# Kernel optimization log

Measured on AMD Instinct MI355X. Metric: run time of the kernel, lower is better.

## Reference

```python
import jax, jax.numpy as jnp
import numpy as np

N = 100000
F_IN = 256
F_OUT = 64
E = 3200000
NEG_SLOPE = 0.2


def setup_inputs() -> dict:
    key = jax.random.key(0)
    k1, k2, k3, k4, k5 = jax.random.split(key, 5)
    x = jax.random.normal(k1, (N, F_IN), dtype=jnp.float32)
    edge_index = jax.random.randint(k2, (2, E), 0, N, dtype=jnp.int32)
    # GATConv params (heads=1): lin weight, att_src, att_dst, bias
    W = jax.random.normal(k3, (F_IN, F_OUT), dtype=jnp.float32) / np.sqrt(F_IN)
    att_src = jax.random.normal(k4, (F_OUT,), dtype=jnp.float32) / np.sqrt(F_OUT)
    att_dst = jax.random.normal(k5, (F_OUT,), dtype=jnp.float32) / np.sqrt(F_OUT)
    bias = jnp.zeros((F_OUT,), dtype=jnp.float32)
    return {"x": x, "edge_index": edge_index, "W": W,
            "att_src": att_src, "att_dst": att_dst, "bias": bias}


def reference(x, edge_index, W, att_src, att_dst, bias):
    n = x.shape[0]
    h = x @ W  # [N, F_OUT]
    # add self-loops (PyG default add_self_loops=True)
    loops = jnp.arange(n, dtype=edge_index.dtype)
    src = jnp.concatenate([edge_index[0], loops])  # message source j
    dst = jnp.concatenate([edge_index[1], loops])  # message target i
    # per-node attention halves
    a_src = h @ att_src  # [N]
    a_dst = h @ att_dst  # [N]
    e = a_src[src] + a_dst[dst]  # [E+N]
    e = jnp.where(e > 0, e, NEG_SLOPE * e)  # LeakyReLU(0.2)
    # softmax over edges grouped by target node
    e_max = jax.ops.segment_max(e, dst, num_segments=n)
    e_max = jnp.where(jnp.isfinite(e_max), e_max, 0.0)
    p = jnp.exp(e - e_max[dst])
    denom = jax.ops.segment_sum(p, dst, num_segments=n)
    alpha = p / (denom[dst] + 1e-16)  # [E+N]
    # scatter-aggregate weighted source features
    out = jax.ops.segment_sum(alpha[:, None] * h[src], dst, num_segments=n)
    return out + bias
```

## Files before the change

kernel.cpp:

```cpp
#include <hip/hip_runtime.h>
#include <hip/hip_bf16.h>
#include <math.h>

#define F_IN 256
#define F_OUT 64
#define NEG_SLOPE 0.2f
#define SHIFT 7
#define NPB 128
#define MAXK 1024
#define CAP 4608
#define OVF 4
#define GRID_B 256

__device__ __forceinline__ float bf2f(__hip_bfloat16 v) {
    return __bfloat162float(v);
}

__global__ __launch_bounds__(256) void gemm_kernel(
    const float* __restrict__ x, const float* __restrict__ W,
    const float* __restrict__ att_src, const float* __restrict__ att_dst,
    __hip_bfloat16* __restrict__ h16, float* __restrict__ a_src,
    float* __restrict__ a_dst, int N)
{
    __shared__ float sX[64][65];
    __shared__ float sPa[4][64];
    __shared__ float sPd[4][64];

    const int t = threadIdx.x;
    const int lane = t & 63;
    const int w = t >> 6;
    const int rowBase = blockIdx.x * 64;
    const int row = rowBase + lane;
    const int c0 = __builtin_amdgcn_readfirstlane(w * 16);

    float acc[16];
#pragma unroll
    for (int c = 0; c < 16; c++) acc[c] = 0.f;

    const int kq = t & 15;
    const int rr = t >> 4;

    for (int kc = 0; kc < F_IN / 64; kc++) {
#pragma unroll
        for (int p = 0; p < 4; p++) {
            int r = rr + p * 16;
            float4 v = make_float4(0.f, 0.f, 0.f, 0.f);
            if (rowBase + r < N)
                v = *(const float4*)&x[(size_t)(rowBase + r) * F_IN + kc * 64 + kq * 4];
            sX[kq * 4 + 0][r] = v.x;
            sX[kq * 4 + 1][r] = v.y;
            sX[kq * 4 + 2][r] = v.z;
            sX[kq * 4 + 3][r] = v.w;
        }
        __syncthreads();

        const float* Wc = W + (size_t)(kc * 64) * F_OUT + c0;
#pragma unroll 4
        for (int kk = 0; kk < 64; kk++) {
            float xv = sX[kk][lane];
            const float* wr = Wc + (size_t)kk * F_OUT;
#pragma unroll
            for (int c = 0; c < 16; c++)
                acc[c] = fmaf(xv, wr[c], acc[c]);
        }
        __syncthreads();
    }

    float asp = 0.f, adp = 0.f;
#pragma unroll
    for (int c = 0; c < 16; c++) {
        asp = fmaf(acc[c], att_src[c0 + c], asp);
        adp = fmaf(acc[c], att_dst[c0 + c], adp);
    }
    sPa[w][lane] = asp;
    sPd[w][lane] = adp;

    if (row < N) {
        __hip_bfloat16 tmp[16];
#pragma unroll
        for (int c = 0; c < 16; c++) tmp[c] = __float2bfloat16(acc[c]);
        int4* dst = (int4*)(h16 + (size_t)row * F_OUT + c0);
        dst[0] = ((int4*)tmp)[0];
        dst[1] = ((int4*)tmp)[1];
    }

    __syncthreads();
    if (w == 0 && row < N) {
        a_src[row] = sPa[0][lane] + sPa[1][lane] + sPa[2][lane] + sPa[3][lane];
        a_dst[row] = sPd[0][lane] + sPd[1][lane] + sPd[2][lane] + sPd[3][lane];
    }
}

__global__ __launch_bounds__(1024) void bucket_count_kernel(
    const int* __restrict__ dst, int* __restrict__ pbh, int E, int K, int R)
{
    __shared__ int s[MAXK];
    const int t = threadIdx.x;
    for (int b = t; b < K; b += 1024) s[b] = 0;
    __syncthreads();
    const int start = blockIdx.x * R;
    const int end = min(E, start + R);
    for (int e = start + t * 4; e < end; e += 4096) {
        if (e + 3 < end) {
            int4 d = *(const int4*)&dst[e];
            atomicAdd(&s[d.x >> SHIFT], 1);
            atomicAdd(&s[d.y >> SHIFT], 1);
            atomicAdd(&s[d.z >> SHIFT], 1);
            atomicAdd(&s[d.w >> SHIFT], 1);
        } else {
            for (int q = e; q < end; q++) atomicAdd(&s[dst[q] >> SHIFT], 1);
        }
    }
    __syncthreads();
    int* row = pbh + (size_t)blockIdx.x * K;
    for (int b = t; b < K; b += 1024) row[b] = s[b];
}

__global__ __launch_bounds__(64) void colscan_kernel(
    const int* __restrict__ pbh, int* __restrict__ cbase,
    int* __restrict__ btot, int K, int NBLK)
{
    const int k = blockIdx.x;
    const int lane = threadIdx.x;
    int v[4];
#pragma unroll
    for (int c = 0; c < 4; c++) {
        int b = c * 64 + lane;
        v[c] = (b < NBLK) ? pbh[(size_t)b * K + k] : 0;
    }
    int carry = 0;
#pragma unroll
    for (int c = 0; c < 4; c++) {
        int orig = v[c];
        int s = v[c];
#pragma unroll
        for (int off = 1; off < 64; off <<= 1) {
            int u = __shfl_up(s, off, 64);
            if (lane >= off) s += u;
        }
        int b = c * 64 + lane;
        if (b < NBLK) cbase[(size_t)b * K + k] = carry + s - orig;
        carry += __shfl(s, 63, 64);
    }
    if (lane == 0) btot[k] = carry;
}

__global__ __launch_bounds__(1024) void bbase_scan_kernel(
    const int* __restrict__ btot, int* __restrict__ bbase, int K, int E)
{
    __shared__ int s[1024];
    const int t = threadIdx.x;
    int v = (t < K) ? btot[t] : 0;
    s[t] = v;
    __syncthreads();
    for (int off = 1; off < 1024; off <<= 1) {
        int u = (t >= off) ? s[t - off] : 0;
        __syncthreads();
        s[t] += u;
        __syncthreads();
    }
    if (t < K) bbase[t] = s[t] - v;
    if (t == 0) bbase[K] = E;
}

__global__ __launch_bounds__(1024) void bin_kernel(
    const int* __restrict__ ei, const int* __restrict__ cbase,
    const int* __restrict__ bbase, int* __restrict__ rec, int E, int K, int R)
{
    __shared__ int cb[MAXK];
    const int t = threadIdx.x;
    const int start = blockIdx.x * R;
    const int end = min(E, start + R);
    const int* crow = cbase + (size_t)blockIdx.x * K;
    for (int b = t; b < K; b += 1024) cb[b] = bbase[b] + crow[b];
    __syncthreads();

    for (int e = start + t * 4; e < end; e += 4096) {
        if (e + 3 < end) {
            int4 jj = *(const int4*)&ei[e];
            int4 ii = *(const int4*)&ei[E + e];
            int p0 = atomicAdd(&cb[ii.x >> SHIFT], 1);
            int p1 = atomicAdd(&cb[ii.y >> SHIFT], 1);
            int p2 = atomicAdd(&cb[ii.z >> SHIFT], 1);
            int p3 = atomicAdd(&cb[ii.w >> SHIFT], 1);
            rec[p0] = jj.x | ((ii.x & (NPB - 1)) << 17);
            rec[p1] = jj.y | ((ii.y & (NPB - 1)) << 17);
            rec[p2] = jj.z | ((ii.z & (NPB - 1)) << 17);
            rec[p3] = jj.w | ((ii.w & (NPB - 1)) << 17);
        } else {
            for (int q = e; q < end; q++) {
                int j = ei[q], i = ei[E + q];
                int pos = atomicAdd(&cb[i >> SHIFT], 1);
                rec[pos] = j | ((i & (NPB - 1)) << 17);
            }
        }
    }
}

__global__ __launch_bounds__(256) void sort_kernel(
    int* __restrict__ rec, const int* __restrict__ bbase,
    int* __restrict__ row_ptr, int N, int E, int K)
{
    __shared__ int stage[CAP];
    __shared__ int deg[NPB];
    __shared__ int sval[NPB];
    __shared__ int base[NPB];
    __shared__ int cnt[NPB];
    const int t = threadIdx.x;
    const int b = blockIdx.x;
    const int s = bbase[b], e = bbase[b + 1];
    const int tot = e - s;
    const int nodeBase = b << SHIFT;
    const int nodes = min(NPB, N - nodeBase);

    if (t < NPB) deg[t] = 0;
    __syncthreads();

    int ovf[OVF];
    for (int r = t; r < tot; r += 256) {
        int m = rec[s + r];
        if (r < CAP) stage[r] = m;
        else { int k = (r - CAP) >> 8; if (k < OVF) ovf[k] = m; }
        atomicAdd(&deg[(m >> 17) & (NPB - 1)], 1);
    }
    __syncthreads();

    if (t < NPB) sval[t] = deg[t];
    __syncthreads();
    for (int off = 1; off < NPB; off <<= 1) {
        int v = (t < NPB && t >= off) ? sval[t - off] : 0;
        __syncthreads();
        if (t < NPB) sval[t] += v;
        __syncthreads();
    }
    if (t < NPB) {
        base[t] = sval[t] - deg[t];
        cnt[t] = 0;
        if (t < nodes) row_ptr[nodeBase + t] = s + base[t];
    }
    if (b == K - 1 && t == 0) row_ptr[N] = E;
    __syncthreads();

    for (int r = t; r < tot; r += 256) {
        int m = (r < CAP) ? stage[r] : ovf[(r - CAP) >> 8];
        int li = (m >> 17) & (NPB - 1);
        int rk = atomicAdd(&cnt[li], 1);
        rec[s + base[li] + rk] = m;
    }
}

__global__ __launch_bounds__(256) void node_kernel(
    const __hip_bfloat16* __restrict__ h16, const float* __restrict__ a_src,
    const float* __restrict__ a_dst, const int* __restrict__ row_ptr,
    const int* __restrict__ rec, const float* __restrict__ bias,
    float* __restrict__ out, int N)
{
    const int w = threadIdx.x >> 6;
    const int lane = threadIdx.x & 63;
    const int i = blockIdx.x * 4 + w;
    if (i >= N) return;

    const int s = row_ptr[i];
    const int e = row_ptr[i + 1];

    const float adst_i = a_dst[i];
    float vs = a_src[i] + adst_i;
    vs = fmaxf(vs, NEG_SLOPE * vs);
    const float pself = __expf(vs);
    float denl = (lane == 0) ? pself : 0.f;
    float acc = pself * bf2f(h16[(size_t)i * F_OUT + lane]);

    for (int k = s; k < e; k += 64) {
        const int cnt = min(64, e - k);
        int r = (lane < cnt) ? rec[k + lane] : 0;
        int j = r & 0x1FFFF;
        float v = a_src[j] + adst_i;
        v = fmaxf(v, NEG_SLOPE * v);
        float p = __expf(v);
        if (lane >= cnt) p = 0.f;
        denl += p;

        int u = 0;
        for (; u + 8 <= cnt; u += 8) {
            int ju[8]; float pu[8], g[8];
#pragma unroll
            for (int c = 0; c < 8; c++) {
                ju[c] = __shfl(j, u + c, 64);
                pu[c] = __shfl(p, u + c, 64);
            }
#pragma unroll
            for (int c = 0; c < 8; c++)
                g[c] = bf2f(h16[(size_t)ju[c] * F_OUT + lane]);
            asm volatile("" ::: "memory");
#pragma unroll
            for (int c = 0; c < 8; c++)
                acc = fmaf(pu[c], g[c], acc);
        }
        for (; u < cnt; u++) {
            int jc = __shfl(j, u, 64);
            float pc = __shfl(p, u, 64);
            acc = fmaf(pc, bf2f(h16[(size_t)jc * F_OUT + lane]), acc);
        }
    }

    float den = denl;
#pragma unroll
    for (int o = 32; o > 0; o >>= 1) den += __shfl_xor(den, o, 64);

    out[(size_t)i * F_OUT + lane] = acc / (den + 1e-16f) + bias[lane];
}

extern "C" void kernel_launch(void* const* d_in, const int* in_sizes, int n_in,
                              void* d_out, int out_size, void* d_ws, size_t ws_size,
                              hipStream_t stream)
{
    const float* x      = (const float*)d_in[0];
    const int*   ei     = (const int*)d_in[1];
    const float* W      = (const float*)d_in[2];
    const float* att_sr = (const float*)d_in[3];
    const float* att_ds = (const float*)d_in[4];
    const float* bias   = (const float*)d_in[5];
    float* out = (float*)d_out;

    const int N = in_sizes[0] / F_IN;
    const int E = in_sizes[1] / 2;
    const int K = (N + NPB - 1) >> SHIFT;
    const int R = (((E + GRID_B - 1) / GRID_B) + 3) & ~3;

    char* ws = (char*)d_ws;
    size_t off = 0;
    auto alloc = [&](size_t bytes) -> void* {
        void* p = ws + off;
        off = (off + bytes + 255) & ~(size_t)255;
        return p;
    };
    __hip_bfloat16* h16 = (__hip_bfloat16*)alloc((size_t)N * F_OUT * 2);
    float* a_src   = (float*)alloc((size_t)N * 4);
    float* a_dst   = (float*)alloc((size_t)N * 4);
    int*   pbh     = (int*)alloc((size_t)GRID_B * K * 4);
    int*   cbase   = (int*)alloc((size_t)GRID_B * K * 4);
    int*   btot    = (int*)alloc((size_t)K * 4);
    int*   bbase   = (int*)alloc((size_t)(K + 1) * 4);
    int*   row_ptr = (int*)alloc((size_t)(N + 1) * 4);
    int*   rec     = (int*)alloc((size_t)E * 4);
    (void)ws_size; (void)n_in; (void)out_size;

    gemm_kernel<<<(N + 63) / 64, 256, 0, stream>>>(x, W, att_sr, att_ds, h16, a_src, a_dst, N);
    bucket_count_kernel<<<GRID_B, 1024, 0, stream>>>(ei + E, pbh, E, K, R);
    colscan_kernel<<<K, 64, 0, stream>>>(pbh, cbase, btot, K, GRID_B);
    bbase_scan_kernel<<<1, 1024, 0, stream>>>(btot, bbase, K, E);
    bin_kernel<<<GRID_B, 1024, 0, stream>>>(ei, cbase, bbase, rec, E, K, R);
    sort_kernel<<<K, 256, 0, stream>>>(rec, bbase, row_ptr, N, E, K);
    node_kernel<<<(N + 3) / 4, 256, 0, stream>>>(h16, a_src, a_dst, row_ptr, rec, bias, out, N);
}
```

Measured before the change: 386.1 us.

## Rewrite projection GEMM with split-bf16 MFMA and persistent tiles

The FP32 scalar-FMA GEMM is replaced by a persistent kernel that emulates FP32 with three bf16 MFMA products (hi*hi, lo*hi, hi*lo). W is split into hi/lo parts once per block and kept in shared memory. Attention dot products are reduced with lane shuffles. The aim is to move the x@W projection onto matrix cores while keeping near-FP32 accuracy. The costs are extra conversion ALU work, 64KB of LDS per block, and h16 stores that are no longer vectorized.

```diff
diff --git a/kernel.cpp b/kernel.cpp
--- a/kernel.cpp
+++ b/kernel.cpp
@@ -16,78 +16,140 @@
     return __bfloat162float(v);
 }
 
-__global__ __launch_bounds__(256) void gemm_kernel(
+typedef short short8 __attribute__((ext_vector_type(8)));
+typedef float f32x4 __attribute__((ext_vector_type(4)));
+
+__device__ __forceinline__ unsigned int bf16_bits(float v) {
+    unsigned int u = __float_as_uint(v);
+    return (u + 0x7fffu + ((u >> 16) & 1u)) >> 16;
+}
+
+#define WHI(q, c, l) (((((q)*4 + (c)) * 64) + (l)) * 8)
+#define WLO(q, c, l) (16384 + WHI(q, c, l))
+
+__global__ __launch_bounds__(256, 2) void gemm_kernel(
     const float* __restrict__ x, const float* __restrict__ W,
     const float* __restrict__ att_src, const float* __restrict__ att_dst,
     __hip_bfloat16* __restrict__ h16, float* __restrict__ a_src,
-    float* __restrict__ a_dst, int N)
-{
-    __shared__ float sX[64][65];
-    __shared__ float sPa[4][64];
-    __shared__ float sPd[4][64];
+    float* __restrict__ a_dst, int N, int nTiles)
+{
+    __shared__ unsigned short sW[32768];
 
     const int t = threadIdx.x;
     const int lane = t & 63;
     const int w = t >> 6;
-    const int rowBase = blockIdx.x * 64;
-    const int row = rowBase + lane;
-    const int c0 = __builtin_amdgcn_readfirstlane(w * 16);
-
-    float acc[16];
-#pragma unroll
-    for (int c = 0; c < 16; c++) acc[c] = 0.f;
-
-    const int kq = t & 15;
-    const int rr = t >> 4;
-
-    for (int kc = 0; kc < F_IN / 64; kc++) {
-#pragma unroll
-        for (int p = 0; p < 4; p++) {
-            int r = rr + p * 16;
-            float4 v = make_float4(0.f, 0.f, 0.f, 0.f);
-            if (rowBase + r < N)
-                v = *(const float4*)&x[(size_t)(rowBase + r) * F_IN + kc * 64 + kq * 4];
-            sX[kq * 4 + 0][r] = v.x;
-            sX[kq * 4 + 1][r] = v.y;
-            sX[kq * 4 + 2][r] = v.z;
-            sX[kq * 4 + 3][r] = v.w;
-        }
-        __syncthreads();
-
-        const float* Wc = W + (size_t)(kc * 64) * F_OUT + c0;
-#pragma unroll 4
-        for (int kk = 0; kk < 64; kk++) {
-            float xv = sX[kk][lane];
-            const float* wr = Wc + (size_t)kk * F_OUT;
-#pragma unroll
-            for (int c = 0; c < 16; c++)
-                acc[c] = fmaf(xv, wr[c], acc[c]);
-        }
-        __syncthreads();
-    }
-
-    float asp = 0.f, adp = 0.f;
-#pragma unroll
-    for (int c = 0; c < 16; c++) {
-        asp = fmaf(acc[c], att_src[c0 + c], asp);
-        adp = fmaf(acc[c], att_dst[c0 + c], adp);
-    }
-    sPa[w][lane] = asp;
-    sPd[w][lane] = adp;
-
-    if (row < N) {
-        __hip_bfloat16 tmp[16];
-#pragma unroll
-        for (int c = 0; c < 16; c++) tmp[c] = __float2bfloat16(acc[c]);
-        int4* dst = (int4*)(h16 + (size_t)row * F_OUT + c0);
-        dst[0] = ((int4*)tmp)[0];
-        dst[1] = ((int4*)tmp)[1];
-    }
-
-    __syncthreads();
-    if (w == 0 && row < N) {
-        a_src[row] = sPa[0][lane] + sPa[1][lane] + sPa[2][lane] + sPa[3][lane];
-        a_dst[row] = sPd[0][lane] + sPd[1][lane] + sPd[2][lane] + sPd[3][lane];
+    const int g = lane >> 4;
+    const int fr = lane & 15;
+
+    for (int idx = t; idx < 2048; idx += 256) {
+        const int q = idx >> 8;
+        const int c = (idx >> 6) & 3;
+        const int l = idx & 63;
+        const int col = c * 16 + (l & 15);
+        const float* wp = W + (size_t)(q * 32 + ((l >> 4) * 8)) * F_OUT + col;
+        short8 hv, lv;
+#pragma unroll
+        for (int e = 0; e < 8; e++) {
+            float wv = wp[(size_t)e * F_OUT];
+            unsigned int hb = bf16_bits(wv);
+            float hf = __uint_as_float(hb << 16);
+            unsigned int lb = bf16_bits(wv - hf);
+            hv[e] = (short)hb;
+            lv[e] = (short)lb;
+        }
+        *(short8*)&sW[WHI(q, c, l)] = hv;
+        *(short8*)&sW[WLO(q, c, l)] = lv;
+    }
+    __syncthreads();
+
+    float as4[4], ad4[4];
+#pragma unroll
+    for (int c = 0; c < 4; c++) {
+        as4[c] = att_src[c * 16 + fr];
+        ad4[c] = att_dst[c * 16 + fr];
+    }
+
+    const float4 z4 = make_float4(0.f, 0.f, 0.f, 0.f);
+
+    for (int tile = blockIdx.x; tile < nTiles; tile += gridDim.x) {
+        const int R0 = tile * 64 + w * 16;
+        const int rowA = R0 + fr;
+        const bool okA = rowA < N;
+        const float* xrow = x + (size_t)rowA * F_IN + g * 8;
+
+        float4 xv[16];
+#pragma unroll
+        for (int q = 0; q < 8; q++) {
+            xv[2 * q]     = okA ? *(const float4*)(xrow + q * 32)     : z4;
+            xv[2 * q + 1] = okA ? *(const float4*)(xrow + q * 32 + 4) : z4;
+        }
+
+        f32x4 acc[4];
+#pragma unroll
+        for (int c = 0; c < 4; c++) acc[c] = (f32x4){0.f, 0.f, 0.f, 0.f};
+
+#pragma unroll
+        for (int q = 0; q < 8; q++) {
+            const float vf[8] = {xv[2 * q].x, xv[2 * q].y, xv[2 * q].z, xv[2 * q].w,
+                                 xv[2 * q + 1].x, xv[2 * q + 1].y, xv[2 * q + 1].z, xv[2 * q + 1].w};
+            short8 ahi, alo;
+#pragma unroll
+            for (int e = 0; e < 8; e++) {
+                unsigned int hb = bf16_bits(vf[e]);
+                float hf = __uint_as_float(hb << 16);
+                unsigned int lb = bf16_bits(vf[e] - hf);
+                ahi[e] = (short)hb;
+                alo[e] = (short)lb;
+            }
+#pragma unroll
+            for (int c = 0; c < 4; c++) {
+                short8 bh = *(const short8*)&sW[WHI(q, c, lane)];
+                short8 bl = *(const short8*)&sW[WLO(q, c, lane)];
+                acc[c] = __builtin_amdgcn_mfma_f32_16x16x32_bf16(ahi, bh, acc[c], 0, 0, 0);
+                acc[c] = __builtin_amdgcn_mfma_f32_16x16x32_bf16(alo, bh, acc[c], 0, 0, 0);
+                acc[c] = __builtin_amdgcn_mfma_f32_16x16x32_bf16(ahi, bl, acc[c], 0, 0, 0);
+            }
+        }
+
+        float sr[4] = {0.f, 0.f, 0.f, 0.f};
+        float sd[4] = {0.f, 0.f, 0.f, 0.f};
+#pragma unroll
+        for (int c = 0; c < 4; c++) {
+#pragma unroll
+            for (int r = 0; r < 4; r++) {
+                float v = acc[c][r];
+                sr[r] = fmaf(v, as4[c], sr[r]);
+                sd[r] = fmaf(v, ad4[c], sd[r]);
+            }
+        }
+#pragma unroll
+        for (int off = 1; off <= 8; off <<= 1) {
+#pragma unroll
+            for (int r = 0; r < 4; r++) {
+                sr[r] += __shfl_xor(sr[r], off, 64);
+                sd[r] += __shfl_xor(sd[r], off, 64);
+            }
+        }
+
+#pragma unroll
+        for (int c = 0; c < 4; c++) {
+#pragma unroll
+            for (int r = 0; r < 4; r++) {
+                const int row = R0 + g * 4 + r;
+                if (row < N)
+                    h16[(size_t)row * F_OUT + c * 16 + fr] = __float2bfloat16(acc[c][r]);
+            }
+        }
+
+        if (fr < 4) {
+            const int row = R0 + g * 4 + fr;
+            if (row < N) {
+                float vs = (fr == 0) ? sr[0] : (fr == 1) ? sr[1] : (fr == 2) ? sr[2] : sr[3];
+                float vd = (fr == 0) ? sd[0] : (fr == 1) ? sd[1] : (fr == 2) ? sd[2] : sd[3];
+                a_src[row] = vs;
+                a_dst[row] = vd;
+            }
+        }
     }
 }
 
@@ -345,7 +407,10 @@
     int*   rec     = (int*)alloc((size_t)E * 4);
     (void)ws_size; (void)n_in; (void)out_size;
 
-    gemm_kernel<<<(N + 63) / 64, 256, 0, stream>>>(x, W, att_sr, att_ds, h16, a_src, a_dst, N);
+    const int nTiles = (N + 63) >> 6;
+    const int gemmGrid = nTiles < 512 ? nTiles : 512;
+
+    gemm_kernel<<<gemmGrid, 256, 0, stream>>>(x, W, att_sr, att_ds, h16, a_src, a_dst, N, nTiles);
     bucket_count_kernel<<<GRID_B, 1024, 0, stream>>>(ei + E, pbh, E, K, R);
     colscan_kernel<<<K, 64, 0, stream>>>(pbh, cbase, btot, K, GRID_B);
     bbase_scan_kernel<<<1, 1024, 0, stream>>>(btot, bbase, K, E);
```

New measurement: 398.6 us. +3.2%, slower.
